# Performance work log

Measured on AMD Instinct MI355X. Metric: run time of the kernel, lower is better.

Reference implementation:

```python
import jax, jax.numpy as jnp
import numpy as np

T = 50          # rollout_len
B = 8192        # batch
FEAT = 14       # idm_s feature dim
CM = 3          # merger context dim
PROJ = 128
DEC = 128
ATT_TEMP = 5.0
DUMMY_DX = 100.0   # dummy_value_set['em_delta_x']
DUMMY_DV = 0.0     # dummy_value_set['em_delta_v']


def setup_inputs() -> dict:
    key = jax.random.key(0)
    ks = jax.random.split(key, 16)
    # IDM params must be positive (sqrt, division); desired_v realistic ~10-30 m/s
    idm_params = jax.random.uniform(ks[0], (B, 5), minval=0.5, maxval=2.0)
    idm_params = idm_params.at[:, 0].set(
        jax.random.uniform(ks[1], (B,), minval=10.0, maxval=30.0))
    proj_latent = jax.random.normal(ks[2], (B, PROJ), dtype=jnp.float32)
    enc_h = jax.random.normal(ks[3], (B, DEC), dtype=jnp.float32)
    idm_s = jax.random.uniform(ks[4], (B, T + 1, FEAT), minval=0.0, maxval=20.0)
    m_exists = (jax.random.uniform(ks[5], (B, T + 1, 1)) > 0.5).astype(jnp.float32)
    idm_s = idm_s.at[:, :, -1:].set(m_exists)
    merger_cs = jax.random.normal(ks[6], (B, T, CM), dtype=jnp.float32)
    scaler_mean = jax.random.normal(ks[7], (8,), dtype=jnp.float32)
    scaler_var = jax.random.uniform(ks[8], (8,), minval=0.5, maxval=2.0)
    IN = PROJ + DEC + 8 + CM  # 267
    s = 0.05
    return {
        'idm_params': idm_params, 'proj_latent': proj_latent, 'enc_h': enc_h,
        'idm_s': idm_s, 'merger_cs': merger_cs,
        'scaler_mean': scaler_mean, 'scaler_var': scaler_var,
        'W1': jax.random.normal(ks[9], (IN, DEC)) * s,
        'b1': jnp.zeros((DEC,), jnp.float32),
        'W2': jax.random.normal(ks[10], (DEC, DEC)) * s,
        'b2': jnp.zeros((DEC,), jnp.float32),
        'Wf': jax.random.normal(ks[11], (DEC, 1)) * s,
        'bf': jnp.zeros((1,), jnp.float32),
        'Wm': jax.random.normal(ks[12], (DEC, 1)) * s,
        'bm': jnp.zeros((1,), jnp.float32),
    }


def _idm_act(vel, dv, dx, p):
    # p: [B,5] = desired_v, desired_tgap, min_jamx, max_act, min_act
    dx = jnp.clip(dx, 0.1, 500.0)
    desired_v, desired_tgap, min_jamx, max_act, min_act = (
        p[:, 0:1], p[:, 1:2], p[:, 2:3], p[:, 3:4], p[:, 4:5])
    gap_denum = 2.0 * jnp.sqrt(max_act * min_act)
    gap = desired_tgap * vel + vel * dv / gap_denum
    desired_gap = min_jamx + jax.nn.relu(gap)
    act = max_act * (1.0 - (vel / desired_v) ** 4 - (desired_gap / dx) ** 2)
    return jnp.clip(act, -6.0, 6.0)


def _rollout(idm_params, proj_latent, enc_h, idm_s, merger_cs,
             scaler_mean, scaler_var, W1, b1, W2, b2, Wf, bf, Wm, bm):
    b = idm_s.shape[0]
    inv_std = 1.0 / jnp.sqrt(scaler_var)

    ego_v = idm_s[:, 0, 0:1]
    ego_a = idm_s[:, 0, 11:12]
    ego_x = idm_s[:, 0, 3:4]
    disp = jnp.zeros((b, 1), jnp.float32)

    def step(carry, xs):
        ego_v, ego_a, ego_x, disp = carry
        s, mc = xs  # s: [B,FEAT], mc: [B,CM]
        f_v = s[:, 1:2]
        m_v = s[:, 2:3]
        f_x = s[:, 4:5]
        m_x = s[:, 5:6]
        f_a = s[:, 12:13]
        m_e = s[:, 13:14]  # m_veh_exists
        ef_dx = f_x - ego_x
        em_dx = (m_x - ego_x) * m_e + (1.0 - m_e) * DUMMY_DX
        ef_dv = ego_v - f_v
        em_dv = (ego_v - m_v) * m_e + (1.0 - m_e) * DUMMY_DV
        env = jnp.concatenate(
            [ego_a, f_a, ego_v, f_v, ef_dv, ef_dx, em_dv, em_dx], axis=-1)
        env = (env - scaler_mean) * inv_std
        h = jnp.concatenate([proj_latent, enc_h, env, mc], axis=-1)  # [B,267]
        h = jax.nn.leaky_relu(h @ W1 + b1, 0.3)
        h = jax.nn.leaky_relu(h @ W2 + b2, 0.3)
        f_sc = jnp.clip(h @ Wf + bf, -20.0, 20.0)
        m_sc = jnp.clip(h @ Wm + bm, -20.0, 20.0)
        fe = jnp.exp(f_sc * ATT_TEMP)
        me = jnp.exp(m_sc * ATT_TEMP)
        tot = fe + me
        f_att = fe / tot
        m_att = me / tot
        ef_act = _idm_act(ego_v, ef_dv, ef_dx, idm_params)
        em_act = _idm_act(ego_v, em_dv, em_dx, idm_params)
        ego_a2 = f_att * ef_act + m_att * em_act
        delta = ego_v * 0.1 + 0.5 * ego_a2 * 0.1 ** 2
        disp2 = disp + delta
        ego_x2 = ego_x + delta
        ego_v2 = ego_v + ego_a2 * 0.1
        return (ego_v2, ego_a2, ego_x2, disp2), (disp2, ego_a2, f_att, m_att)

    xs = (jnp.swapaxes(idm_s[:, :T, :], 0, 1),    # [T,B,FEAT]
          jnp.swapaxes(merger_cs, 0, 1))          # [T,B,CM]
    _, (disp_seq, act_seq, f_att_seq, m_att_seq) = jax.lax.scan(
        step, (ego_v, ego_a, ego_x, disp), xs)
    # [T,B,1] -> [B,T,1]
    disp_seq = jnp.swapaxes(disp_seq, 0, 1)
    act_seq = jnp.swapaxes(act_seq, 0, 1)
    f_att_seq = jnp.swapaxes(f_att_seq, 0, 1)
    m_att_seq = jnp.swapaxes(m_att_seq, 0, 1)
    disp_seq = jnp.concatenate(
        [jnp.zeros((b, 1, 1), jnp.float32), disp_seq], axis=1)  # [B,T+1,1]
    return disp_seq, act_seq, f_att_seq, m_att_seq


def reference(idm_params, proj_latent, enc_h, idm_s, merger_cs,
              scaler_mean, scaler_var, W1, b1, W2, b2, Wf, bf, Wm, bm):
    return _rollout(idm_params, proj_latent, enc_h, idm_s, merger_cs,
                    scaler_mean, scaler_var, W1, b1, W2, b2, Wf, bf, Wm, bm)
```

## Files before the change

kernel.cpp:

```cpp
#include <hip/hip_runtime.h>

#define NB 8192
#define NT 50

typedef _Float16 half8 __attribute__((ext_vector_type(8)));
typedef float f32x4 __attribute__((ext_vector_type(4)));

__device__ __forceinline__ float leaky(float x) { return x > 0.0f ? x : 0.3f * x; }
__device__ __forceinline__ float frcp(float x) { return __builtin_amdgcn_rcpf(x); }

#define LVL_SCALE   4096.0f
#define LVL_UNSCALE 0.000244140625f

extern "C" __global__ __launch_bounds__(256, 2)
void idm_rollout_kernel(const float* __restrict__ idm_params,
                        const float* __restrict__ proj_latent,
                        const float* __restrict__ enc_h,
                        const float* __restrict__ idm_s,
                        const float* __restrict__ merger_cs,
                        const float* __restrict__ scaler_mean,
                        const float* __restrict__ scaler_var,
                        const float* __restrict__ W1,
                        const float* __restrict__ b1,
                        const float* __restrict__ W2,
                        const float* __restrict__ b2,
                        const float* __restrict__ Wf,
                        const float* __restrict__ bfp,
                        const float* __restrict__ Wm,
                        const float* __restrict__ bmp,
                        float* __restrict__ out)
{
    __shared__ __align__(16) _Float16 s_a[4][2][64][8];
    __shared__ __align__(16) float s_w1d[11][128];
    __shared__ __align__(16) float s_part[16][12];

    const int tid = threadIdx.x;
    const int w   = tid >> 6;
    const int l   = tid & 63;
    const int lm  = l & 15;
    const int lq  = l >> 4;
    const int b0  = blockIdx.x * 16;
    const int bm  = b0 + lm;
    const int c0  = w * 32 + lq * 8;

    for (int idx = tid; idx < 11 * 128; idx += 256) {
        const int r = idx >> 7, c = idx & 127;
        float wv_ = W1[(256 + r) * 128 + c];
        if (r < 8) wv_ *= 1.0f / sqrtf(scaler_var[r]);
        s_w1d[r][c] = wv_;
    }

    half8 W2T0[2][4], W2T1[2][4];
    #pragma unroll
    for (int jt = 0; jt < 2; ++jt) {
        const int jtg = 2 * w + jt;
        #pragma unroll
        for (int kc = 0; kc < 4; ++kc) {
            #pragma unroll
            for (int e = 0; e < 8; ++e) {
                const int k = kc * 32 + lq * 8 + e;
                const float v = W2[k * 128 + jtg * 16 + lm];
                const _Float16 q0 = (_Float16)v;
                const float r1 = (v - (float)q0) * LVL_SCALE;
                W2T0[jt][kc][e] = q0;
                W2T1[jt][kc][e] = (_Float16)r1;
            }
        }
    }

    f32x4 b2r[2], wfr[2], wmr[2];
    #pragma unroll
    for (int jt = 0; jt < 2; ++jt) {
        const int cb = (2 * w + jt) * 16 + lq * 4;
        b2r[jt] = *(const f32x4*)&b2[cb];
        wfr[jt] = *(const f32x4*)&Wf[cb];
        wmr[jt] = *(const f32x4*)&Wm[cb];
    }
    const float bfv = bfp[0];
    const float bmv = bmp[0];

    __syncthreads();

    f32x4 hpA = *(const f32x4*)&b1[c0];
    f32x4 hpB = *(const f32x4*)&b1[c0 + 4];
    {
        const float* xl0 = proj_latent + (size_t)bm * 128;
        const float* xl1 = enc_h + (size_t)bm * 128;
        #pragma unroll 2
        for (int r0 = 0; r0 < 128; r0 += 4) {
            const f32x4 x = *(const f32x4*)&xl0[r0];
            #pragma unroll
            for (int j = 0; j < 4; ++j) {
                hpA += x[j] * *(const f32x4*)&W1[(r0 + j) * 128 + c0];
                hpB += x[j] * *(const f32x4*)&W1[(r0 + j) * 128 + c0 + 4];
            }
        }
        #pragma unroll 2
        for (int r0 = 0; r0 < 128; r0 += 4) {
            const f32x4 x = *(const f32x4*)&xl1[r0];
            #pragma unroll
            for (int j = 0; j < 4; ++j) {
                hpA += x[j] * *(const f32x4*)&W1[(128 + r0 + j) * 128 + c0];
                hpB += x[j] * *(const f32x4*)&W1[(128 + r0 + j) * 128 + c0 + 4];
            }
        }
        #pragma unroll
        for (int rr = 0; rr < 8; ++rr) {
            const float c = scaler_mean[rr];
            hpA -= c * *(const f32x4*)&s_w1d[rr][c0];
            hpB -= c * *(const f32x4*)&s_w1d[rr][c0 + 4];
        }
    }

    float ego_v_r, ego_a_r, ego_x_r, disp_r;
    float ef_dv_r, ef_dx_r, em_dv_r, em_dx_r;
    float c_fa, c_fv, c_m0, c_m1, c_m2;
    {
        const float* sr = idm_s + (size_t)bm * 714;
        const float* mr = merger_cs + (size_t)bm * 150;
        ego_v_r = sr[0]; ego_a_r = sr[11]; ego_x_r = sr[3]; disp_r = 0.0f;
        const float fv0 = sr[1], mv0 = sr[2], fx0 = sr[4], mx0 = sr[5];
        c_fa = sr[12];
        const float me0 = sr[13];
        c_fv = fv0;
        ef_dx_r = fx0 - ego_x_r;
        em_dx_r = (mx0 - ego_x_r) * me0 + (1.0f - me0) * 100.0f;
        ef_dv_r = ego_v_r - fv0;
        em_dv_r = (ego_v_r - mv0) * me0;
        c_m0 = mr[0]; c_m1 = mr[1]; c_m2 = mr[2];
    }
    const float ptg    = idm_params[bm * 5 + 1];
    const float pjam   = idm_params[bm * 5 + 2];
    const float pamax  = idm_params[bm * 5 + 3];
    const float pinv_v0 = 1.0f / idm_params[bm * 5 + 0];
    const float pinv_gd = 1.0f / (2.0f * sqrtf(pamax * idm_params[bm * 5 + 4]));

    float* out_disp = out;
    float* out_act  = out + NB * 51;
    float* out_fat  = out + NB * (51 + 50);
    float* out_mat  = out + NB * (51 + 100);
    if (tid < 16) out_disp[bm * 51] = 0.0f;

    for (int t = 0; t < NT; ++t) {
        float nf_fv = 0, nf_mv = 0, nf_fx = 0, nf_mx = 0, nf_fa = 0, nf_me = 0;
        float nf_m0 = 0, nf_m1 = 0, nf_m2 = 0;
        if (t + 1 < NT) {
            const float* sp = idm_s + (size_t)bm * 714 + (t + 1) * 14;
            nf_fv = sp[1]; nf_mv = sp[2]; nf_fx = sp[4]; nf_mx = sp[5];
            nf_fa = sp[12]; nf_me = sp[13];
            const float* mp = merger_cs + (size_t)bm * 150 + (t + 1) * 3;
            nf_m0 = mp[0]; nf_m1 = mp[1]; nf_m2 = mp[2];
        }

        float ev[11];
        ev[0] = ego_a_r; ev[1] = c_fa;    ev[2] = ego_v_r; ev[3] = c_fv;
        ev[4] = ef_dv_r; ev[5] = ef_dx_r; ev[6] = em_dv_r; ev[7] = em_dx_r;
        ev[8] = c_m0;    ev[9] = c_m1;    ev[10] = c_m2;
        f32x4 hqA = hpA, hqB = hpB;
        #pragma unroll
        for (int r = 0; r < 11; ++r) {
            hqA += ev[r] * *(const f32x4*)&s_w1d[r][c0];
            hqB += ev[r] * *(const f32x4*)&s_w1d[r][c0 + 4];
        }
        float h[8];
        h[0] = leaky(hqA.x); h[1] = leaky(hqA.y); h[2] = leaky(hqA.z); h[3] = leaky(hqA.w);
        h[4] = leaky(hqB.x); h[5] = leaky(hqB.y); h[6] = leaky(hqB.z); h[7] = leaky(hqB.w);

        half8 A0, A1;
        #pragma unroll
        for (int e = 0; e < 8; ++e) {
            const float v = h[e];
            const _Float16 q0 = (_Float16)v;
            A0[e] = q0;
            A1[e] = (_Float16)((v - (float)q0) * LVL_SCALE);
        }
        *(half8*)&s_a[w][0][l][0] = A0;
        *(half8*)&s_a[w][1][l][0] = A1;

        __syncthreads();

        f32x4 aA[2], aB[2], aC[2];
        #pragma unroll
        for (int jt = 0; jt < 2; ++jt) {
            aA[jt] = f32x4{0,0,0,0}; aB[jt] = f32x4{0,0,0,0}; aC[jt] = f32x4{0,0,0,0};
        }
        #pragma unroll
        for (int kc = 0; kc < 4; ++kc) {
            const half8 x0 = *(const half8*)&s_a[kc][0][l][0];
            const half8 x1 = *(const half8*)&s_a[kc][1][l][0];
            #pragma unroll
            for (int jt = 0; jt < 2; ++jt) {
                aA[jt] = __builtin_amdgcn_mfma_f32_16x16x32_f16(W2T0[jt][kc], x0, aA[jt], 0, 0, 0);
                aB[jt] = __builtin_amdgcn_mfma_f32_16x16x32_f16(W2T1[jt][kc], x0, aB[jt], 0, 0, 0);
                aC[jt] = __builtin_amdgcn_mfma_f32_16x16x32_f16(W2T0[jt][kc], x1, aC[jt], 0, 0, 0);
            }
        }
        float fsc = 0.0f, msc = 0.0f;
        #pragma unroll
        for (int jt = 0; jt < 2; ++jt) {
            #pragma unroll
            for (int r = 0; r < 4; ++r) {
                const float h2 = leaky(aA[jt][r] + (aB[jt][r] + aC[jt][r]) * LVL_UNSCALE
                                       + b2r[jt][r]);
                fsc += h2 * wfr[jt][r];
                msc += h2 * wmr[jt][r];
            }
        }
        fsc += __shfl_xor(fsc, 16); fsc += __shfl_xor(fsc, 32);
        msc += __shfl_xor(msc, 16); msc += __shfl_xor(msc, 32);
        if (l < 16) *(float2*)&s_part[lm][w * 2] = make_float2(fsc, msc);

        __syncthreads();

        {
            const f32x4 p0 = *(const f32x4*)&s_part[lm][0];
            const f32x4 p1 = *(const f32x4*)&s_part[lm][4];
            const float fsum = bfv + p0.x + p0.z + p1.x + p1.z;
            const float msum = bmv + p0.y + p0.w + p1.y + p1.w;

            const float f_sc = fminf(fmaxf(fsum, -20.0f), 20.0f);
            const float m_sc = fminf(fmaxf(msum, -20.0f), 20.0f);
            const float dsc = 5.0f * (f_sc - m_sc);
            const float ex  = __expf(-fabsf(dsc));
            const float inv = frcp(1.0f + ex);
            const float fatt = (dsc >= 0.0f) ? inv : ex * inv;
            const float matt = 1.0f - fatt;

            const float rr_ = ego_v_r * pinv_v0;
            const float rr2 = rr_ * rr_;
            const float base = pamax * (1.0f - rr2 * rr2);
            const float dxf = fminf(fmaxf(ef_dx_r, 0.1f), 500.0f);
            const float gapf = ptg * ego_v_r + ego_v_r * ef_dv_r * pinv_gd;
            const float dgf = pjam + fmaxf(gapf, 0.0f);
            const float qf = dgf * frcp(dxf);
            const float efa = fminf(fmaxf(base - pamax * qf * qf, -6.0f), 6.0f);
            const float dxm = fminf(fmaxf(em_dx_r, 0.1f), 500.0f);
            const float gapm = ptg * ego_v_r + ego_v_r * em_dv_r * pinv_gd;
            const float dgm = pjam + fmaxf(gapm, 0.0f);
            const float qm = dgm * frcp(dxm);
            const float ema = fminf(fmaxf(base - pamax * qm * qm, -6.0f), 6.0f);

            const float a2n = fatt * efa + matt * ema;

            const float delta = ego_v_r * 0.1f + 0.005f * a2n;
            disp_r  += delta;
            ego_x_r += delta;
            ego_v_r += a2n * 0.1f;
            ego_a_r  = a2n;

            if (tid < 16) {
                out_disp[bm * 51 + t + 1] = disp_r;
                out_act [bm * 50 + t]     = a2n;
                out_fat [bm * 50 + t]     = fatt;
                out_mat [bm * 50 + t]     = matt;
            }

            if (t + 1 < NT) {
                ef_dx_r = nf_fx - ego_x_r;
                em_dx_r = (nf_mx - ego_x_r) * nf_me + (1.0f - nf_me) * 100.0f;
                ef_dv_r = ego_v_r - nf_fv;
                em_dv_r = (ego_v_r - nf_mv) * nf_me;
                c_fa = nf_fa; c_fv = nf_fv;
                c_m0 = nf_m0; c_m1 = nf_m1; c_m2 = nf_m2;
            }
        }
    }
}

extern "C" void kernel_launch(void* const* d_in, const int* in_sizes, int n_in,
                              void* d_out, int out_size, void* d_ws, size_t ws_size,
                              hipStream_t stream) {
    (void)in_sizes; (void)n_in; (void)d_ws; (void)ws_size; (void)out_size;
    const float* idm_params  = (const float*)d_in[0];
    const float* proj_latent = (const float*)d_in[1];
    const float* enc_h       = (const float*)d_in[2];
    const float* idm_s       = (const float*)d_in[3];
    const float* merger_cs   = (const float*)d_in[4];
    const float* scaler_mean = (const float*)d_in[5];
    const float* scaler_var  = (const float*)d_in[6];
    const float* W1          = (const float*)d_in[7];
    const float* b1          = (const float*)d_in[8];
    const float* W2          = (const float*)d_in[9];
    const float* b2          = (const float*)d_in[10];
    const float* Wf          = (const float*)d_in[11];
    const float* bfp         = (const float*)d_in[12];
    const float* Wm          = (const float*)d_in[13];
    const float* bmp         = (const float*)d_in[14];

    idm_rollout_kernel<<<dim3(NB / 16), dim3(256), 0, stream>>>(
        idm_params, proj_latent, enc_h, idm_s, merger_cs,
        scaler_mean, scaler_var, W1, b1, W2, b2, Wf, bfp, Wm, bmp,
        (float*)d_out);
}
```

Baseline: 154.1 us.

## Stage per-step inputs and outputs in shared memory with coalesced bulk transfers

Before the time loop, the block now preloads all future per-step idm_s features and merger context for its 16 batch rows into shared memory, replacing strided per-step global loads issued inside the serial recurrence. Per-step outputs are buffered in shared memory and written out coalesced after the loop. m_att is reconstructed as 1 - f_att rather than stored. The cost is a larger shared-memory footprint, which can lower occupancy under the launch bounds.

Result: faster. 132.8 us (-13.8%).

```diff
diff --git a/kernel.cpp b/kernel.cpp
--- a/kernel.cpp
+++ b/kernel.cpp
@@ -33,6 +33,9 @@
     __shared__ __align__(16) _Float16 s_a[4][2][64][8];
     __shared__ __align__(16) float s_w1d[11][128];
     __shared__ __align__(16) float s_part[16][12];
+    __shared__ __align__(16) float s_tA[50][16][8];
+    __shared__ __align__(16) float s_tB[50][16][4];
+    __shared__ float s_out[16][151];
 
     const int tid = threadIdx.x;
     const int w   = tid >> 6;
@@ -49,6 +52,22 @@
         if (r < 8) wv_ *= 1.0f / sqrtf(scaler_var[r]);
         s_w1d[r][c] = wv_;
     }
+    for (int idx = tid; idx < 16 * 49 * 6; idx += 256) {
+        const int e  = idx / 294;
+        const int r2 = idx - e * 294;
+        const int tt = r2 / 6;
+        const int s  = r2 - tt * 6;
+        const int col = (s < 2) ? (s + 1) : ((s < 4) ? (s + 2) : (s + 8));
+        s_tA[tt][e][s] = idm_s[(size_t)(b0 + e) * 714 + (tt + 1) * 14 + col];
+    }
+    for (int idx = tid; idx < 16 * 49 * 3; idx += 256) {
+        const int e  = idx / 147;
+        const int r2 = idx - e * 147;
+        const int tt = r2 / 3;
+        const int s  = r2 - tt * 3;
+        s_tB[tt][e][s] = merger_cs[(size_t)(b0 + e) * 150 + (tt + 1) * 3 + s];
+    }
+    if (tid < 16) s_out[tid][0] = 0.0f;
 
     half8 W2T0[2][4], W2T1[2][4];
     #pragma unroll
@@ -135,23 +154,7 @@
     const float pinv_v0 = 1.0f / idm_params[bm * 5 + 0];
     const float pinv_gd = 1.0f / (2.0f * sqrtf(pamax * idm_params[bm * 5 + 4]));
 
-    float* out_disp = out;
-    float* out_act  = out + NB * 51;
-    float* out_fat  = out + NB * (51 + 50);
-    float* out_mat  = out + NB * (51 + 100);
-    if (tid < 16) out_disp[bm * 51] = 0.0f;
-
     for (int t = 0; t < NT; ++t) {
-        float nf_fv = 0, nf_mv = 0, nf_fx = 0, nf_mx = 0, nf_fa = 0, nf_me = 0;
-        float nf_m0 = 0, nf_m1 = 0, nf_m2 = 0;
-        if (t + 1 < NT) {
-            const float* sp = idm_s + (size_t)bm * 714 + (t + 1) * 14;
-            nf_fv = sp[1]; nf_mv = sp[2]; nf_fx = sp[4]; nf_mx = sp[5];
-            nf_fa = sp[12]; nf_me = sp[13];
-            const float* mp = merger_cs + (size_t)bm * 150 + (t + 1) * 3;
-            nf_m0 = mp[0]; nf_m1 = mp[1]; nf_m2 = mp[2];
-        }
-
         float ev[11];
         ev[0] = ego_a_r; ev[1] = c_fa;    ev[2] = ego_v_r; ev[3] = c_fv;
         ev[4] = ef_dv_r; ev[5] = ef_dx_r; ev[6] = em_dv_r; ev[7] = em_dx_r;
@@ -178,6 +181,10 @@
         *(half8*)&s_a[w][1][l][0] = A1;
 
         __syncthreads();
+
+        const f32x4  ta = *(const f32x4*)&s_tA[t][lm][0];
+        const float2 tb = *(const float2*)&s_tA[t][lm][4];
+        const f32x4  tc = *(const f32x4*)&s_tB[t][lm][0];
 
         f32x4 aA[2], aB[2], aC[2];
         #pragma unroll
@@ -249,21 +256,35 @@
             ego_a_r  = a2n;
 
             if (tid < 16) {
-                out_disp[bm * 51 + t + 1] = disp_r;
-                out_act [bm * 50 + t]     = a2n;
-                out_fat [bm * 50 + t]     = fatt;
-                out_mat [bm * 50 + t]     = matt;
+                s_out[lm][t + 1]   = disp_r;
+                s_out[lm][51 + t]  = a2n;
+                s_out[lm][101 + t] = fatt;
             }
 
             if (t + 1 < NT) {
-                ef_dx_r = nf_fx - ego_x_r;
-                em_dx_r = (nf_mx - ego_x_r) * nf_me + (1.0f - nf_me) * 100.0f;
-                ef_dv_r = ego_v_r - nf_fv;
-                em_dv_r = (ego_v_r - nf_mv) * nf_me;
-                c_fa = nf_fa; c_fv = nf_fv;
-                c_m0 = nf_m0; c_m1 = nf_m1; c_m2 = nf_m2;
-            }
-        }
+                ef_dx_r = ta.z - ego_x_r;
+                em_dx_r = (ta.w - ego_x_r) * tb.y + (1.0f - tb.y) * 100.0f;
+                ef_dv_r = ego_v_r - ta.x;
+                em_dv_r = (ego_v_r - ta.y) * tb.y;
+                c_fa = tb.x; c_fv = ta.x;
+                c_m0 = tc.x; c_m1 = tc.y; c_m2 = tc.z;
+            }
+        }
+    }
+
+    __syncthreads();
+    float* out_disp = out;
+    float* out_act  = out + NB * 51;
+    float* out_fat  = out + NB * (51 + 50);
+    float* out_mat  = out + NB * (51 + 100);
+    for (int idx = tid; idx < 16 * 51; idx += 256)
+        out_disp[b0 * 51 + idx] = s_out[idx / 51][idx % 51];
+    for (int idx = tid; idx < 16 * 50; idx += 256) {
+        const int e = idx / 50, t = idx % 50;
+        out_act[b0 * 50 + idx] = s_out[e][51 + t];
+        const float f = s_out[e][101 + t];
+        out_fat[b0 * 50 + idx] = f;
+        out_mat[b0 * 50 + idx] = 1.0f - f;
     }
 }
 
```
